# Kernel tuning notes

Measured on AMD Instinct MI355X. Metric: run time of the kernel, lower is better.

The kernel has to match this reference:

```python
import jax, jax.numpy as jnp
import numpy as np

EMBED = 1024
HEADS = 16
HEAD_DIM = EMBED // HEADS
NEG = -1e20


def setup_inputs() -> dict:
    key = jax.random.key(0)
    ks = jax.random.split(key, 12)
    N, S, E = 2, 2048, EMBED
    w = lambda k: (jax.random.normal(k, (E, E), dtype=jnp.float32) * 0.02)
    b = lambda k: (jax.random.normal(k, (E,), dtype=jnp.float32) * 0.02)
    return {
        "values": jax.random.normal(ks[0], (N, S, E), dtype=jnp.float32),
        "keys": jax.random.normal(ks[1], (N, S, E), dtype=jnp.float32),
        "query": jax.random.normal(ks[2], (N, S, E), dtype=jnp.float32),
        "mask": jnp.ones((N, S), dtype=jnp.int32),
        "Wv": w(ks[3]), "bv": b(ks[4]),
        "Wk": w(ks[5]), "bk": b(ks[6]),
        "Wq": w(ks[7]), "bq": b(ks[8]),
        "Wo": w(ks[9]), "bo": b(ks[10]),
    }


def reference(values, keys, query, mask, Wv, bv, Wk, bk, Wq, bq, Wo, bo):
    N, S, E = query.shape
    # torch nn.Linear: x @ W.T + b
    v = (values @ Wv.T + bv).reshape(N, S, HEADS, HEAD_DIM)
    k = (keys @ Wk.T + bk).reshape(N, S, HEADS, HEAD_DIM)
    q = (query @ Wq.T + bq).reshape(N, S, HEADS, HEAD_DIM)
    # full [N,H,Q,K] score matrix, as in the original einsum
    energy = jnp.einsum('nqhd,nkhd->nhqk', q, k)
    # 2D mask with mismatched dims triggers causal tril path in the original
    causal = jnp.tril(jnp.ones((S, S), dtype=bool))  # [Q,K]
    energy = jnp.where(causal[None, None, :, :], energy, NEG)
    # NOTE: original scales by sqrt(embed_size), not sqrt(head_dim)
    attn = jax.nn.softmax(energy / jnp.sqrt(jnp.float32(E)), axis=3)
    out = jnp.einsum('nhqk,nkhd->nqhd', attn, v).reshape(N, S, E)
    return out @ Wo.T + bo
```

## Files before the change

### kernel.cpp

```cpp
#include <hip/hip_runtime.h>

typedef __bf16 bf16;
typedef __bf16 bf16x4 __attribute__((ext_vector_type(4)));
typedef __bf16 bf16x8 __attribute__((ext_vector_type(8)));
typedef float floatx4 __attribute__((ext_vector_type(4)));

#define GLOAD_LDS16(gp, lp) \
  __builtin_amdgcn_global_load_lds( \
      (const __attribute__((address_space(1))) void*)(gp), \
      (__attribute__((address_space(3))) void*)(lp), 16, 0, 0)

__global__ __launch_bounds__(256) void cvt_all_kernel(
    const float* __restrict__ v, const float* __restrict__ k, const float* __restrict__ q,
    const float* __restrict__ wv, const float* __restrict__ wk,
    const float* __restrict__ wq, const float* __restrict__ wo,
    bf16* __restrict__ xv, bf16* __restrict__ xk, bf16* __restrict__ xq,
    bf16* __restrict__ bwv, bf16* __restrict__ bwk, bf16* __restrict__ bwq,
    bf16* __restrict__ bwo) {
  const int i = blockIdx.x * 256 + threadIdx.x;
  const int A4 = 1 << 20;
  const float* src; bf16* dst; int off;
  if (i < A4)            { src = v; dst = xv; off = i; }
  else if (i < 2 * A4)   { src = k; dst = xk; off = i - A4; }
  else if (i < 3 * A4)   { src = q; dst = xq; off = i - 2 * A4; }
  else {
    int j = i - 3 * A4; int r = j >> 18; off = j & ((1 << 18) - 1);
    src = (r == 0) ? wv : (r == 1) ? wk : (r == 2) ? wq : wo;
    dst = (r == 0) ? bwv : (r == 1) ? bwk : (r == 2) ? bwq : bwo;
  }
  float4 x = reinterpret_cast<const float4*>(src)[off];
  union { bf16 b[4]; short4 s; } u;
  u.b[0] = (bf16)x.x; u.b[1] = (bf16)x.y; u.b[2] = (bf16)x.z; u.b[3] = (bf16)x.w;
  reinterpret_cast<short4*>(dst)[off] = u.s;
}

template <int MODE>
__device__ __forceinline__ void gemm_body(
    const bf16* __restrict__ A, const bf16* __restrict__ B,
    const float* __restrict__ bias, void* __restrict__ Cout) {
  constexpr int K = 1024, N = 1024;
  __shared__ __align__(16) bf16 As[128 * 32];
  __shared__ __align__(16) bf16 Bs[128 * 32];
  const int tid = threadIdx.x;
  const int lane = tid & 63;
  const int wave = tid >> 6;
  const int quad = lane >> 4;
  const int l16 = lane & 15;
  const int wm = (wave >> 1) * 64;
  const int wn = (wave & 1) * 64;
  const int am0 = blockIdx.y * 128;
  const int bn0 = blockIdx.x * 128;
  const int srow = lane >> 2;
  const int scol = (lane & 3) * 8;

  floatx4 acc[4][4] = {};

  for (int k0 = 0; k0 < K; k0 += 32) {
    __syncthreads();
#pragma unroll
    for (int j = 0; j < 2; j++) {
      const int chunk = wave * 2 + j;
      const int row = chunk * 16 + srow;
      GLOAD_LDS16(A + (size_t)(am0 + row) * K + k0 + scol, As + chunk * 512);
      GLOAD_LDS16(B + (size_t)(bn0 + row) * K + k0 + scol, Bs + chunk * 512);
    }
    __syncthreads();

    bf16x8 af[4], bfv[4];
#pragma unroll
    for (int mi = 0; mi < 4; mi++)
      af[mi] = *reinterpret_cast<const bf16x8*>(&As[(wm + mi * 16 + l16) * 32 + quad * 8]);
#pragma unroll
    for (int ni = 0; ni < 4; ni++)
      bfv[ni] = *reinterpret_cast<const bf16x8*>(&Bs[(wn + ni * 16 + l16) * 32 + quad * 8]);
#pragma unroll
    for (int mi = 0; mi < 4; mi++)
#pragma unroll
      for (int ni = 0; ni < 4; ni++)
        acc[mi][ni] = __builtin_amdgcn_mfma_f32_16x16x32_bf16(af[mi], bfv[ni], acc[mi][ni], 0, 0, 0);
  }

#pragma unroll
  for (int mi = 0; mi < 4; mi++) {
#pragma unroll
    for (int ni = 0; ni < 4; ni++) {
      const int col = bn0 + wn + ni * 16 + l16;
      const float bb = bias[col];
      const int row = am0 + wm + mi * 16 + quad * 4;
      if constexpr (MODE == 2) {
#pragma unroll
        for (int r = 0; r < 4; r++)
          reinterpret_cast<float*>(Cout)[(size_t)(row + r) * N + col] = acc[mi][ni][r] + bb;
      } else {
        const int nb = row >> 11;
        const int s = row & 2047;
        const int h = col >> 6;
        const int d = col & 63;
        const int nh = nb * 16 + h;
        if constexpr (MODE == 0) {
          bf16* base = reinterpret_cast<bf16*>(Cout) + ((size_t)nh * 2048 + s) * 64 + d;
#pragma unroll
          for (int r = 0; r < 4; r++) base[(size_t)r * 64] = (bf16)(acc[mi][ni][r] + bb);
        } else {
          bf16x4 pk;
#pragma unroll
          for (int r = 0; r < 4; r++) pk[r] = (bf16)(acc[mi][ni][r] + bb);
          *reinterpret_cast<bf16x4*>(
              reinterpret_cast<bf16*>(Cout) + ((size_t)nh * 64 + d) * 2048 + s) = pk;
        }
      }
    }
  }
}

__global__ __launch_bounds__(256) void gemm_qkv(
    const bf16* __restrict__ A0, const bf16* __restrict__ B0, const float* __restrict__ c0, bf16* __restrict__ C0,
    const bf16* __restrict__ A1, const bf16* __restrict__ B1, const float* __restrict__ c1, bf16* __restrict__ C1,
    const bf16* __restrict__ A2, const bf16* __restrict__ B2, const float* __restrict__ c2, bf16* __restrict__ C2) {
  if (blockIdx.z == 0)      gemm_body<0>(A0, B0, c0, C0);
  else if (blockIdx.z == 1) gemm_body<0>(A1, B1, c1, C1);
  else                      gemm_body<1>(A2, B2, c2, C2);
}

__global__ __launch_bounds__(256) void gemm_out(
    const bf16* __restrict__ A, const bf16* __restrict__ B,
    const float* __restrict__ bias, float* __restrict__ C) {
  gemm_body<2>(A, B, bias, C);
}

#define S_LEN 2048
#define EMB 1024
#define QT 128
#define KTILE 64
#define PSTR 72
#define SCALE2 (0.03125f * 1.44269504f)

__global__ __launch_bounds__(256) void attn_kernel(
    const bf16* __restrict__ Qh, const bf16* __restrict__ Kh,
    const bf16* __restrict__ Vt, bf16* __restrict__ O) {
  __shared__ __align__(16) bf16 Ps[QT * PSTR];

  const int tid = threadIdx.x;
  const int lane = tid & 63;
  const int wave = tid >> 6;
  const int quad = lane >> 4;
  const int l16 = lane & 15;
  const int wq = wave * 32;

  const int id = blockIdx.x;
  const int p = id & 255;
  const int half = id >> 8;
  const int qtl = p & 7;
  const int qt = half ? (15 - qtl) : qtl;
  const int nh = p >> 3;
  const int n = nh >> 4;
  const int h = nh & 15;
  const int q0 = qt * QT;

  bf16x8 aq[2][2];
  {
    const bf16* Qb = Qh + ((size_t)nh * S_LEN + q0 + wq + l16) * 64 + quad * 8;
#pragma unroll
    for (int mi = 0; mi < 2; mi++)
#pragma unroll
      for (int kc = 0; kc < 2; kc++)
        aq[mi][kc] = *reinterpret_cast<const bf16x8*>(Qb + mi * 16 * 64 + kc * 32);
  }

  float l_part[2][4] = {};
  floatx4 o_acc[2][4] = {};

  const bf16* Kb = Kh + ((size_t)nh * S_LEN + l16) * 64 + quad * 8;
  const bf16* Vb = Vt + ((size_t)nh * 64 + l16) * S_LEN + quad * 8;

  bf16x8 kb[2][2][4];

#pragma unroll
  for (int kc = 0; kc < 2; kc++)
#pragma unroll
    for (int ni = 0; ni < 4; ni++)
      kb[0][kc][ni] = *reinterpret_cast<const bf16x8*>(Kb + (size_t)(ni * 16) * 64 + kc * 32);

  auto step = [&](int k0, bf16x8 (&kcur)[2][4], bf16x8 (&knx)[2][4], int k0n) {
    bf16x8 vb[2][4];
#pragma unroll
    for (int kc = 0; kc < 2; kc++)
#pragma unroll
      for (int di = 0; di < 4; di++)
        vb[kc][di] = *reinterpret_cast<const bf16x8*>(Vb + (size_t)(di * 16) * S_LEN + k0 + kc * 32);
#pragma unroll
    for (int kc = 0; kc < 2; kc++)
#pragma unroll
      for (int ni = 0; ni < 4; ni++)
        knx[kc][ni] = *reinterpret_cast<const bf16x8*>(Kb + (size_t)(k0n + ni * 16) * 64 + kc * 32);

    floatx4 s_acc[2][4] = {};
#pragma unroll
    for (int kc = 0; kc < 2; kc++)
#pragma unroll
      for (int mi = 0; mi < 2; mi++)
#pragma unroll
        for (int ni = 0; ni < 4; ni++)
          s_acc[mi][ni] = __builtin_amdgcn_mfma_f32_16x16x32_bf16(aq[mi][kc], kcur[kc][ni], s_acc[mi][ni], 0, 0, 0);

    const bool needMask = (k0 + KTILE - 1) > (q0 + wq);
#pragma unroll
    for (int mi = 0; mi < 2; mi++) {
#pragma unroll
      for (int ni = 0; ni < 4; ni++) {
        const int cg = k0 + ni * 16 + l16;
#pragma unroll
        for (int r = 0; r < 4; r++) {
          const int rg = q0 + wq + mi * 16 + quad * 4 + r;
          float pr = __builtin_amdgcn_exp2f(s_acc[mi][ni][r] * SCALE2);
          if (needMask) pr = (cg <= rg) ? pr : 0.f;
          s_acc[mi][ni][r] = pr;
          l_part[mi][r] += pr;
        }
      }
    }

#pragma unroll
    for (int mi = 0; mi < 2; mi++) {
#pragma unroll
      for (int ni = 0; ni < 4; ni++) {
        const int cl = ni * 2 + (l16 >> 3);
        const int pc = (cl ^ quad) * 8 + (l16 & 7);
#pragma unroll
        for (int r = 0; r < 4; r++)
          Ps[(wq + mi * 16 + quad * 4 + r) * PSTR + pc] = (bf16)s_acc[mi][ni][r];
      }
    }

#pragma unroll
    for (int kc = 0; kc < 2; kc++) {
      bf16x8 ap[2];
      const int pc = ((kc * 4 + quad) ^ (l16 >> 2)) * 8;
#pragma unroll
      for (int mi = 0; mi < 2; mi++)
        ap[mi] = *reinterpret_cast<const bf16x8*>(&Ps[(wq + mi * 16 + l16) * PSTR + pc]);
#pragma unroll
      for (int mi = 0; mi < 2; mi++)
#pragma unroll
        for (int di = 0; di < 4; di++)
          o_acc[mi][di] = __builtin_amdgcn_mfma_f32_16x16x32_bf16(ap[mi], vb[kc][di], o_acc[mi][di], 0, 0, 0);
    }
  };

  const int ktiles = 2 * qt + 2;
  for (int kt = 0; kt < ktiles; kt += 2) {
    const int k0a = kt * KTILE;
    const int k0b = k0a + KTILE;
    const int k0c = (kt + 2 < ktiles) ? (kt + 2) * KTILE : 0;
    step(k0a, kb[0], kb[1], k0b);
    step(k0b, kb[1], kb[0], k0c);
  }

#pragma unroll
  for (int mi = 0; mi < 2; mi++)
#pragma unroll
    for (int r = 0; r < 4; r++) {
      float s = l_part[mi][r];
#pragma unroll
      for (int off = 1; off < 16; off <<= 1) s += __shfl_xor(s, off);
      l_part[mi][r] = 1.0f / s;
    }

  bf16* Op = O + ((size_t)(n * S_LEN + q0 + wq)) * EMB + h * 64;
#pragma unroll
  for (int mi = 0; mi < 2; mi++) {
#pragma unroll
    for (int r = 0; r < 4; r++) {
      const float inv = l_part[mi][r];
      bf16* orow = Op + (size_t)(mi * 16 + quad * 4 + r) * EMB;
#pragma unroll
      for (int di = 0; di < 4; di++)
        orow[di * 16 + l16] = (bf16)(o_acc[mi][di][r] * inv);
    }
  }
}

extern "C" void kernel_launch(void* const* d_in, const int* in_sizes, int n_in,
                              void* d_out, int out_size, void* d_ws, size_t ws_size,
                              hipStream_t stream) {
  (void)in_sizes; (void)n_in; (void)out_size; (void)ws_size;
  const float* values = (const float*)d_in[0];
  const float* keys   = (const float*)d_in[1];
  const float* query  = (const float*)d_in[2];
  const float* Wv = (const float*)d_in[4];
  const float* bv = (const float*)d_in[5];
  const float* Wk = (const float*)d_in[6];
  const float* bk = (const float*)d_in[7];
  const float* Wq = (const float*)d_in[8];
  const float* bq = (const float*)d_in[9];
  const float* Wo = (const float*)d_in[10];
  const float* bo = (const float*)d_in[11];
  float* out = (float*)d_out;

  const int NB = 2, S = 2048, E = 1024;
  const int M = NB * S;
  const size_t MB_ = 1u << 20;
  char* ws = (char*)d_ws;
  bf16* xv  = (bf16*)(ws + 0 * MB_);
  bf16* xk  = (bf16*)(ws + 8 * MB_);
  bf16* xq  = (bf16*)(ws + 16 * MB_);
  bf16* wvb = (bf16*)(ws + 24 * MB_);
  bf16* wkb = (bf16*)(ws + 26 * MB_);
  bf16* wqb = (bf16*)(ws + 28 * MB_);
  bf16* wob = (bf16*)(ws + 30 * MB_);
  bf16* kh  = (bf16*)(ws + 32 * MB_);
  bf16* qh  = (bf16*)(ws + 40 * MB_);
  bf16* vt  = (bf16*)(ws + 48 * MB_);
  bf16* ao  = (bf16*)(ws + 56 * MB_);

  cvt_all_kernel<<<(4 << 20) / 256, 256, 0, stream>>>(
      values, keys, query, Wv, Wk, Wq, Wo,
      xv, xk, xq, wvb, wkb, wqb, wob);

  gemm_qkv<<<dim3(E / 128, M / 128, 3), 256, 0, stream>>>(
      xq, wqb, bq, qh,
      xk, wkb, bk, kh,
      xv, wvb, bv, vt);

  attn_kernel<<<dim3(512), 256, 0, stream>>>(qh, kh, vt, ao);

  gemm_out<<<dim3(E / 128, M / 128), 256, 0, stream>>>(ao, wob, bo, out);
}
```

Measured before the change: 254.9 us.

## Stage K and V tiles in LDS via direct global-to-LDS loads

Replaces per-wave direct global loads of K and V (with register double buffering of K) by cooperative block-wide staging of each 64-key K and V tile into swizzled shared memory using global_load_lds. All four waves then read their MFMA operands from LDS. This removes the four-fold redundant global traffic, since every wave previously loaded the same K/V tile. In exchange it adds two block barriers per tile and drops the register prefetch, so load latency is no longer overlapped with compute.

```diff
diff --git a/kernel.cpp b/kernel.cpp
--- a/kernel.cpp
+++ b/kernel.cpp
@@ -138,6 +138,8 @@
 __global__ __launch_bounds__(256) void attn_kernel(
     const bf16* __restrict__ Qh, const bf16* __restrict__ Kh,
     const bf16* __restrict__ Vt, bf16* __restrict__ O) {
+  __shared__ __align__(16) bf16 Ks[KTILE * 64];
+  __shared__ __align__(16) bf16 Vs[64 * KTILE];
   __shared__ __align__(16) bf16 Ps[QT * PSTR];
 
   const int tid = threadIdx.x;
@@ -170,38 +172,40 @@
   float l_part[2][4] = {};
   floatx4 o_acc[2][4] = {};
 
-  const bf16* Kb = Kh + ((size_t)nh * S_LEN + l16) * 64 + quad * 8;
-  const bf16* Vb = Vt + ((size_t)nh * 64 + l16) * S_LEN + quad * 8;
-
-  bf16x8 kb[2][2][4];
-
-#pragma unroll
-  for (int kc = 0; kc < 2; kc++)
-#pragma unroll
-    for (int ni = 0; ni < 4; ni++)
-      kb[0][kc][ni] = *reinterpret_cast<const bf16x8*>(Kb + (size_t)(ni * 16) * 64 + kc * 32);
-
-  auto step = [&](int k0, bf16x8 (&kcur)[2][4], bf16x8 (&knx)[2][4], int k0n) {
-    bf16x8 vb[2][4];
-#pragma unroll
-    for (int kc = 0; kc < 2; kc++)
-#pragma unroll
-      for (int di = 0; di < 4; di++)
-        vb[kc][di] = *reinterpret_cast<const bf16x8*>(Vb + (size_t)(di * 16) * S_LEN + k0 + kc * 32);
-#pragma unroll
-    for (int kc = 0; kc < 2; kc++)
+  const bf16* Kbase = Kh + (size_t)nh * S_LEN * 64;
+  const bf16* Vbase = Vt + (size_t)nh * 64 * S_LEN;
+
+  const int srl = lane >> 3;
+  const int sc8 = lane & 7;
+
+  const int ktiles = 2 * qt + 2;
+  for (int kt = 0; kt < ktiles; kt++) {
+    const int k0 = kt * KTILE;
+
+    __syncthreads();
+#pragma unroll
+    for (int j = 0; j < 2; j++) {
+      const int rl = wave * 16 + j * 8 + srl;
+      const int c8 = ((sc8 ^ (rl & 7)) * 8);
+      GLOAD_LDS16(Kbase + (size_t)(k0 + rl) * 64 + c8, Ks + (wave * 16 + j * 8) * 64);
+      GLOAD_LDS16(Vbase + (size_t)rl * S_LEN + k0 + c8, Vs + (wave * 16 + j * 8) * 64);
+    }
+    __syncthreads();
+
+    floatx4 s_acc[2][4] = {};
+#pragma unroll
+    for (int kc = 0; kc < 2; kc++) {
+      bf16x8 bk[4];
 #pragma unroll
       for (int ni = 0; ni < 4; ni++)
-        knx[kc][ni] = *reinterpret_cast<const bf16x8*>(Kb + (size_t)(k0n + ni * 16) * 64 + kc * 32);
-
-    floatx4 s_acc[2][4] = {};
-#pragma unroll
-    for (int kc = 0; kc < 2; kc++)
+        bk[ni] = *reinterpret_cast<const bf16x8*>(
+            &Ks[(ni * 16 + l16) * 64 + (((kc * 4 + quad) ^ (l16 & 7)) * 8)]);
 #pragma unroll
       for (int mi = 0; mi < 2; mi++)
 #pragma unroll
         for (int ni = 0; ni < 4; ni++)
-          s_acc[mi][ni] = __builtin_amdgcn_mfma_f32_16x16x32_bf16(aq[mi][kc], kcur[kc][ni], s_acc[mi][ni], 0, 0, 0);
+          s_acc[mi][ni] = __builtin_amdgcn_mfma_f32_16x16x32_bf16(aq[mi][kc], bk[ni], s_acc[mi][ni], 0, 0, 0);
+    }
 
     const bool needMask = (k0 + KTILE - 1) > (q0 + wq);
 #pragma unroll
@@ -234,26 +238,21 @@
 
 #pragma unroll
     for (int kc = 0; kc < 2; kc++) {
-      bf16x8 ap[2];
+      bf16x8 ap[2], bv[4];
       const int pc = ((kc * 4 + quad) ^ (l16 >> 2)) * 8;
 #pragma unroll
       for (int mi = 0; mi < 2; mi++)
         ap[mi] = *reinterpret_cast<const bf16x8*>(&Ps[(wq + mi * 16 + l16) * PSTR + pc]);
 #pragma unroll
+      for (int di = 0; di < 4; di++)
+        bv[di] = *reinterpret_cast<const bf16x8*>(
+            &Vs[(di * 16 + l16) * 64 + (((kc * 4 + quad) ^ (l16 & 7)) * 8)]);
+#pragma unroll
       for (int mi = 0; mi < 2; mi++)
 #pragma unroll
         for (int di = 0; di < 4; di++)
-          o_acc[mi][di] = __builtin_amdgcn_mfma_f32_16x16x32_bf16(ap[mi], vb[kc][di], o_acc[mi][di], 0, 0, 0);
-    }
-  };
-
-  const int ktiles = 2 * qt + 2;
-  for (int kt = 0; kt < ktiles; kt += 2) {
-    const int k0a = kt * KTILE;
-    const int k0b = k0a + KTILE;
-    const int k0c = (kt + 2 < ktiles) ? (kt + 2) * KTILE : 0;
-    step(k0a, kb[0], kb[1], k0b);
-    step(k0b, kb[1], kb[0], k0c);
+          o_acc[mi][di] = __builtin_amdgcn_mfma_f32_16x16x32_bf16(ap[mi], bv[di], o_acc[mi][di], 0, 0, 0);
+    }
   }
 
 #pragma unroll
```

Result: faster. 239.6 us (-6.0%).
